# Performance work log

Measured on AMD Instinct MI355X. Metric: run time of the kernel, lower is better.

Reference implementation:

```python
import jax, jax.numpy as jnp
import numpy as np

N = 100000   # nodes
E = 300000   # edges per snapshot
S = 5        # snapshots
D_IN = 128   # node_dim
H = 256      # hidden dim
P = 10000    # post nodes


def setup_inputs() -> dict:
    key = jax.random.key(0)
    ks = jax.random.split(key, 8)
    node_features = jax.random.normal(ks[0], (N, D_IN), jnp.float32)
    edge_index = jax.random.randint(ks[1], (S, 2, E), 0, N, dtype=jnp.int64)
    post_idx = jax.random.randint(ks[2], (P,), 0, N, dtype=jnp.int64)
    glorot = lambda k, sh, fan: jax.random.normal(k, sh, jnp.float32) * (1.0 / np.sqrt(fan))
    return {
        'node_features': node_features,
        'edge_index': edge_index,
        'post_idx': post_idx,
        'W1': glorot(ks[3], (D_IN, H), D_IN), 'b1': jnp.zeros((H,), jnp.float32),
        'W2': glorot(ks[4], (H, H), H),       'b2': jnp.zeros((H,), jnp.float32),
        'Wc1': glorot(ks[5], (H, H // 2), H), 'bc1': jnp.zeros((H // 2,), jnp.float32),
        'Wc2': glorot(ks[6], (H // 2, 1), H // 2), 'bc2': jnp.zeros((1,), jnp.float32),
    }


def gcn_conv(x, src, dst, W, b):
    """PyG GCNConv: h = D^-1/2 (A+I) D^-1/2 (x W) + b, aggregate at target (dst)."""
    n = x.shape[0]
    h = x @ W                                   # [n, out]
    loop = jnp.arange(n, dtype=src.dtype)
    src2 = jnp.concatenate([src, loop])          # add self-loops
    dst2 = jnp.concatenate([dst, loop])
    deg = jax.ops.segment_sum(jnp.ones_like(dst2, jnp.float32), dst2, num_segments=n)
    dinv = jnp.where(deg > 0, jax.lax.rsqrt(deg), 0.0)
    norm = dinv[src2] * dinv[dst2]               # [E+n]
    out = jax.ops.segment_sum(h[src2] * norm[:, None], dst2, num_segments=n)
    return out + b


def reference(node_features, edge_index, post_idx, W1, b1, W2, b2, Wc1, bc1, Wc2, bc2):
    embs = []
    for s in range(edge_index.shape[0]):  # loop over fixed small snapshot count
        src, dst = edge_index[s, 0], edge_index[s, 1]
        # layer 0: 128 -> 256, relu, no skip (dims differ)
        x1 = jax.nn.relu(gcn_conv(node_features, src, dst, W1, b1))
        # layer 1 (last): 256 -> 256, no relu, residual skip
        x2 = gcn_conv(x1, src, dst, W2, b2) + x1
        embs.append(x2)
    agg = jnp.mean(jnp.stack(embs, axis=0), axis=0)  # mean over snapshots
    post = agg[post_idx]                             # [P, H]
    logits = jax.nn.relu(post @ Wc1 + bc1) @ Wc2 + bc2
    return jax.nn.sigmoid(logits[:, 0])              # [P]
```

## Files before the change

### kernel.cpp

```cpp
#include <hip/hip_runtime.h>
#include <hip/hip_bf16.h>
#include <math.h>

#define NN 100000
#define NE 300000
#define NS 5
#define DIN 128
#define HID 256
#define NP 10000
#define NB_N 391

#define NBUCK 1024
#define NBUCK_USED 782
#define PBLK 64
#define EPB 19
#define BCAP 2048
#define CAPR 40960
#define NCPAD 16

typedef short s8v __attribute__((ext_vector_type(8)));
typedef float f4v __attribute__((ext_vector_type(4)));

static __device__ __forceinline__ float bf2f(unsigned short u) {
    union { unsigned int i; float f; } v; v.i = ((unsigned int)u) << 16; return v.f;
}
static __device__ __forceinline__ unsigned short f2bf(float f) {
    union { float f; unsigned int i; } v; v.f = f;
    return (unsigned short)((v.i + 0x7fff + ((v.i >> 16) & 1)) >> 16);
}


__global__ void setpost_kernel(const int* __restrict__ post, int* __restrict__ isPost,
                               int* __restrict__ needed) {
    int i = blockIdx.x * 256 + threadIdx.x;
    int s = blockIdx.y;
    if (i < NP) {
        int nd = post[i];
        needed[(size_t)s * NN + nd] = 1;
        if (s == 0) isPost[nd] = 1;
    }
}


__global__ void hist_kernel(const int* __restrict__ EI, int* __restrict__ bhist) {
    __shared__ int h[NBUCK];
    int s = blockIdx.y, b = blockIdx.x, t = threadIdx.x;
    for (int q = t; q < NBUCK; q += 256) h[q] = 0;
    __syncthreads();
    const int* dstp = EI + (size_t)s * 2 * NE + NE;
    int e0 = b * (EPB * 256);
    #pragma unroll
    for (int j = 0; j < EPB; j++) {
        int e = e0 + j * 256 + t;
        if (e < NE) atomicAdd(&h[dstp[e] >> 7], 1);
    }
    __syncthreads();
    for (int q = t; q < NBUCK; q += 256)
        if (h[q]) atomicAdd(&bhist[s * NBUCK + q], h[q]);
}

__global__ void bscan_kernel(const int* __restrict__ bhist, int* __restrict__ bbase,
                             int* __restrict__ bcur) {
    __shared__ int sm[NBUCK];
    int s = blockIdx.x, t = threadIdx.x;
    int v = bhist[s * NBUCK + t];
    sm[t] = v;
    __syncthreads();
    for (int d = 1; d < NBUCK; d <<= 1) {
        int x = (t >= d) ? sm[t - d] : 0;
        __syncthreads();
        sm[t] += x;
        __syncthreads();
    }
    int base = sm[t] - v;
    bbase[s * NBUCK + t] = base;
    bcur[s * NBUCK + t] = base;
}

__global__ void part_kernel(const int* __restrict__ EI, int* __restrict__ bcur,
                            int2* __restrict__ pairs) {
    __shared__ int h[NBUCK];
    __shared__ int base[NBUCK];
    int s = blockIdx.y, b = blockIdx.x, t = threadIdx.x;
    for (int q = t; q < NBUCK; q += 256) h[q] = 0;
    __syncthreads();
    const int* srcp = EI + (size_t)s * 2 * NE;
    const int* dstp = srcp + NE;
    int e0 = b * (EPB * 256);
    int rs[EPB], rd[EPB];
    #pragma unroll
    for (int j = 0; j < EPB; j++) {
        int e = e0 + j * 256 + t;
        if (e < NE) {
            rs[j] = srcp[e];
            rd[j] = dstp[e];
            atomicAdd(&h[rd[j] >> 7], 1);
        } else {
            rd[j] = -1; rs[j] = 0;
        }
    }
    __syncthreads();
    for (int q = t; q < NBUCK; q += 256) {
        int c = h[q];
        base[q] = c ? atomicAdd(&bcur[s * NBUCK + q], c) : 0;
    }
    __syncthreads();
    #pragma unroll
    for (int j = 0; j < EPB; j++) {
        if (rd[j] >= 0) {
            int pos = atomicAdd(&base[rd[j] >> 7], 1);
            pairs[(size_t)s * NE + pos] = make_int2(rs[j], rd[j]);
        }
    }
}

__global__ void bucket_csr_kernel(const int2* __restrict__ pairs, const int* __restrict__ bbase,
                                  const int* __restrict__ bhist, const int* __restrict__ isPost,
                                  int* __restrict__ cnt, int* __restrict__ offs,
                                  float* __restrict__ dinv, int* __restrict__ csr,
                                  int* __restrict__ needed) {
    __shared__ int nh[128];
    __shared__ int noff[128];
    __shared__ int sbuf[BCAP];
    int s = blockIdx.y, b = blockIdx.x, t = threadIdx.x;
    int base = bbase[s * NBUCK + b];
    int count = bhist[s * NBUCK + b];
    if (count > BCAP) count = BCAP;
    if (t < 128) nh[t] = 0;
    __syncthreads();
    const int2* pp = pairs + (size_t)s * NE + base;
    for (int e = t; e < count; e += 256)
        atomicAdd(&nh[pp[e].y & 127], 1);
    __syncthreads();
    if (t < 128) noff[t] = nh[t];
    __syncthreads();
    for (int d = 1; d < 128; d <<= 1) {
        int x = 0;
        if (t < 128 && t >= d) x = noff[t - d];
        __syncthreads();
        if (t < 128) noff[t] += x;
        __syncthreads();
    }
    if (t < 128) {
        int excl = noff[t] - nh[t];
        noff[t] = excl;
        int g = b * 128 + t;
        if (g < NN) {
            int c = nh[t];
            cnt[(size_t)s * NN + g]  = c;
            offs[(size_t)s * NN + g] = base + excl;
            dinv[(size_t)s * NN + g] = rsqrtf((float)(c + 1));
        }
    }
    __syncthreads();
    for (int e = t; e < count; e += 256) {
        int2 pr = pp[e];
        int pos = atomicAdd(&noff[pr.y & 127], 1);
        sbuf[pos] = pr.x;
        if (isPost[pr.y]) needed[(size_t)s * NN + pr.x] = 1;
    }
    __syncthreads();
    for (int e = t; e < count; e += 256)
        csr[(size_t)s * NE + base + e] = sbuf[e];
}


__global__ void compact_kernel(const int* __restrict__ needed, int* __restrict__ ncount,
                               int* __restrict__ list, int* __restrict__ inv) {
    __shared__ int wcnt[4];
    __shared__ int gbase;
    int s = blockIdx.y;
    int i = blockIdx.x * 256 + threadIdx.x;
    int wave = threadIdx.x >> 6, lane = threadIdx.x & 63;
    bool pred = (i < NN) && (needed[(size_t)s * NN + i] != 0);
    unsigned long long mask = __ballot(pred);
    int wc = __popcll(mask);
    if (lane == 0) wcnt[wave] = wc;
    __syncthreads();
    if (threadIdx.x == 0) {
        int tot = wcnt[0] + wcnt[1] + wcnt[2] + wcnt[3];
        gbase = tot ? atomicAdd(&ncount[s * NCPAD], tot) : 0;
    }
    __syncthreads();
    if (pred) {
        int wbase = gbase;
        #pragma unroll
        for (int q = 0; q < 4; q++) if (q < wave) wbase += wcnt[q];
        int rank = __popcll(mask & ((1ull << lane) - 1ull));
        int slot = wbase + rank;
        if (slot < CAPR) {
            list[(size_t)s * NN + slot] = i;
            inv[(size_t)s * NN + i] = slot;
        }
    }
}


__global__ void cvt_kernel(const float* __restrict__ src, unsigned short* __restrict__ dstp, int n4) {
    int i = blockIdx.x * 256 + threadIdx.x;
    if (i < n4) {
        float4 v = *(const float4*)&src[(size_t)i * 4];
        ushort4 o;
        o.x = f2bf(v.x); o.y = f2bf(v.y); o.z = f2bf(v.z); o.w = f2bf(v.w);
        *(ushort4*)&dstp[(size_t)i * 4] = o;
    }
}

__global__ void tw_kernel(const float* __restrict__ W, unsigned short* __restrict__ Wt,
                          int K, int Ncols) {
    int i = blockIdx.x * 256 + threadIdx.x;
    if (i < K * Ncols) {
        int n = i / K, k = i - n * K;
        Wt[i] = f2bf(W[(size_t)k * Ncols + n]);
    }
}


__global__ __launch_bounds__(512) void agg_mm1_kernel(
        const unsigned short* __restrict__ Xb, const unsigned short* __restrict__ W1t,
        const int* __restrict__ ncount, const float* __restrict__ dinvA,
        const int* __restrict__ offsA, const int* __restrict__ cntA,
        const int* __restrict__ csrA, const int* __restrict__ listA,
        const float* __restrict__ b1, unsigned short* __restrict__ x1cA) {
    int s = blockIdx.y;
    int M = ncount[s * NCPAD];
    if (M > CAPR) M = CAPR;
    if (blockIdx.x * 128 >= M) return;
    const float* dinv = dinvA + (size_t)s * NN;
    const int* offs = offsA + (size_t)s * NN;
    const int* cnt  = cntA + (size_t)s * NN;
    const int* csr  = csrA + (size_t)s * NE;
    const int* list = listA + (size_t)s * NN;
    unsigned short* x1c = x1cA + (size_t)s * CAPR * HID;

    __shared__ unsigned short ldsB[256 * 136];
    int tid = threadIdx.x;
    for (int q = tid; q < 256 * 16; q += 512) {
        int n = q >> 4;
        int k8 = (q & 15) * 8;
        *(s8v*)&ldsB[n * 136 + k8] = *(const s8v*)&W1t[n * 128 + k8];
    }
    __syncthreads();

    int wave = tid >> 6, lane = tid & 63, lr = lane & 15, g = lane >> 4;
    int rowbase = blockIdx.x * 128 + wave * 16;
    int arow = rowbase + lr;

    float ga[4][8];
    #pragma unroll
    for (int kk = 0; kk < 4; kk++)
        #pragma unroll
        for (int j = 0; j < 8; j++) ga[kk][j] = 0.f;
    float di = 0.f;

    if (arow < M) {
        int node = list[arow];
        int o = offs[node], c = cnt[node];
        di = dinv[node];
        const unsigned short* rp = Xb + (size_t)node * DIN + g * 8;
        #pragma unroll
        for (int kk = 0; kk < 4; kk++) {
            s8v h = *(const s8v*)(rp + kk * 32);
            #pragma unroll
            for (int j = 0; j < 8; j++) ga[kk][j] = di * bf2f((unsigned short)h[j]);
        }
        for (int k = 0; k < c; k++) {
            int sv = csr[o + k];
            float wgt = dinv[sv];
            const unsigned short* sp = Xb + (size_t)sv * DIN + g * 8;
            #pragma unroll
            for (int kk = 0; kk < 4; kk++) {
                s8v h = *(const s8v*)(sp + kk * 32);
                #pragma unroll
                for (int j = 0; j < 8; j++) ga[kk][j] += wgt * bf2f((unsigned short)h[j]);
            }
        }
    }

    f4v acc[16];
    #pragma unroll
    for (int t8 = 0; t8 < 16; t8++) acc[t8] = (f4v){0.f, 0.f, 0.f, 0.f};
    #pragma unroll
    for (int kk = 0; kk < 4; kk++) {
        s8v a;
        #pragma unroll
        for (int j = 0; j < 8; j++) a[j] = (short)f2bf(ga[kk][j]);
        #pragma unroll
        for (int t8 = 0; t8 < 16; t8++) {
            s8v b = *(const s8v*)&ldsB[(t8 * 16 + lr) * 136 + kk * 32 + g * 8];
            acc[t8] = __builtin_amdgcn_mfma_f32_16x16x32_bf16(a, b, acc[t8], 0, 0, 0);
        }
    }

    int orow0 = rowbase + g * 4;
    #pragma unroll
    for (int r = 0; r < 4; r++) {
        int row = orow0 + r;
        float sc = __shfl(di, g * 4 + r, 64);
        if (row < M) {
            #pragma unroll
            for (int t8 = 0; t8 < 16; t8++) {
                int col = t8 * 16 + lr;
                float v = sc * acc[t8][r] + b1[col];
                x1c[(size_t)row * HID + col] = f2bf(v > 0.f ? v : 0.f);
            }
        }
    }
}


__global__ void z2_kernel(const unsigned short* __restrict__ x1cA, const float* __restrict__ dinvA,
                          const int* __restrict__ offsA, const int* __restrict__ cntA,
                          const int* __restrict__ csrA, const int* __restrict__ invA,
                          const int* __restrict__ post, unsigned short* __restrict__ z2bA) {
    int s = blockIdx.y;
    const unsigned short* x1c = x1cA + (size_t)s * CAPR * HID;
    const float* dinv = dinvA + (size_t)s * NN;
    const int* offs = offsA + (size_t)s * NN;
    const int* cnt  = cntA + (size_t)s * NN;
    const int* csr  = csrA + (size_t)s * NE;
    const int* inv  = invA + (size_t)s * NN;
    unsigned short* z2b = z2bA + (size_t)s * NP * HID;

    int wave = threadIdx.x >> 6, lane = threadIdx.x & 63;
    int eg = lane >> 4, el = lane & 15;
    int p = blockIdx.x * 4 + wave;
    if (p >= NP) return;
    int node = post[p];
    int o = offs[node], c = cnt[node];
    float acc0[8] = {0.f, 0.f, 0.f, 0.f, 0.f, 0.f, 0.f, 0.f};
    float acc1[8] = {0.f, 0.f, 0.f, 0.f, 0.f, 0.f, 0.f, 0.f};
    for (int k = eg; k < c; k += 4) {
        int sv = csr[o + k];
        float wgt = dinv[sv];
        int r = inv[sv];
        const unsigned short* rp = &x1c[(size_t)r * HID + el * 16];
        s8v h0 = *(const s8v*)rp;
        s8v h1 = *(const s8v*)(rp + 8);
        #pragma unroll
        for (int j = 0; j < 8; j++) {
            acc0[j] += wgt * bf2f((unsigned short)h0[j]);
            acc1[j] += wgt * bf2f((unsigned short)h1[j]);
        }
    }
    if (eg == 0) {
        float di = dinv[node];
        int r = inv[node];
        const unsigned short* rp = &x1c[(size_t)r * HID + el * 16];
        s8v h0 = *(const s8v*)rp;
        s8v h1 = *(const s8v*)(rp + 8);
        #pragma unroll
        for (int j = 0; j < 8; j++) {
            acc0[j] += di * bf2f((unsigned short)h0[j]);
            acc1[j] += di * bf2f((unsigned short)h1[j]);
        }
    }
    #pragma unroll
    for (int j = 0; j < 8; j++) {
        acc0[j] += __shfl_xor(acc0[j], 16, 64);
        acc0[j] += __shfl_xor(acc0[j], 32, 64);
        acc1[j] += __shfl_xor(acc1[j], 16, 64);
        acc1[j] += __shfl_xor(acc1[j], 32, 64);
    }
    if (eg == 0) {
        s8v o0, o1;
        #pragma unroll
        for (int j = 0; j < 8; j++) {
            o0[j] = (short)f2bf(acc0[j]);
            o1[j] = (short)f2bf(acc1[j]);
        }
        unsigned short* wp = &z2b[(size_t)p * HID + el * 16];
        *(s8v*)wp = o0;
        *(s8v*)(wp + 8) = o1;
    }
}


__global__ __launch_bounds__(512) void mm2_kernel(
        const unsigned short* __restrict__ z2bA,
        const unsigned short* __restrict__ W2t,
        const float* __restrict__ dinvA,
        const int* __restrict__ post,
        const int* __restrict__ invA,
        const float* __restrict__ b2,
        const unsigned short* __restrict__ x1cA,
        float* __restrict__ aggPA) {
    int s = blockIdx.z;
    const unsigned short* A = z2bA + (size_t)s * NP * HID;
    const float* dinv = dinvA + (size_t)s * NN;
    const int* inv = invA + (size_t)s * NN;
    const unsigned short* x1c = x1cA + (size_t)s * CAPR * HID;
    float* Out = aggPA + (size_t)s * NP * HID;

    __shared__ unsigned short lds[128 * (HID + 8)];
    int tid = threadIdx.x;
    int colbase = blockIdx.y * 128;
    for (int q = tid; q < 128 * 32; q += 512) {
        int n = q >> 5;
        int k8 = (q & 31) * 8;
        *(s8v*)&lds[n * (HID + 8) + k8] = *(const s8v*)&W2t[(size_t)(colbase + n) * HID + k8];
    }
    __syncthreads();

    int wave = tid >> 6, lane = tid & 63, lr = lane & 15, g = lane >> 4;
    int rowbase = blockIdx.x * 128 + wave * 16;
    int arow = rowbase + lr;

    f4v acc[8];
    #pragma unroll
    for (int t = 0; t < 8; t++) acc[t] = (f4v){0.f, 0.f, 0.f, 0.f};

    #pragma unroll
    for (int kk = 0; kk < HID / 32; kk++) {
        s8v a = (s8v){0, 0, 0, 0, 0, 0, 0, 0};
        if (arow < NP) a = *(const s8v*)&A[(size_t)arow * HID + kk * 32 + g * 8];
        #pragma unroll
        for (int t = 0; t < 8; t++) {
            s8v b = *(const s8v*)&lds[(t * 16 + lr) * (HID + 8) + kk * 32 + g * 8];
            acc[t] = __builtin_amdgcn_mfma_f32_16x16x32_bf16(a, b, acc[t], 0, 0, 0);
        }
    }

    int orow0 = rowbase + g * 4;
    #pragma unroll
    for (int r = 0; r < 4; r++) {
        int row = orow0 + r;
        if (row < NP) {
            int nd = post[row];
            float sc = dinv[nd];
            size_t x1row = (size_t)inv[nd] * HID;
            #pragma unroll
            for (int t = 0; t < 8; t++) {
                int col = colbase + t * 16 + lr;
                Out[(size_t)row * HID + col] =
                    sc * acc[t][r] + b2[col] + bf2f(x1c[x1row + col]);
            }
        }
    }
}


__global__ void redcvt_kernel(const float* __restrict__ aggPA, unsigned short* __restrict__ aggPb) {
    int i = blockIdx.x * 256 + threadIdx.x;
    if (i < NP * HID / 4) {
        float4 a = *(const float4*)&aggPA[(size_t)i * 4];
        #pragma unroll
        for (int s = 1; s < NS; s++) {
            float4 b = *(const float4*)&aggPA[(size_t)s * NP * HID + (size_t)i * 4];
            a.x += b.x; a.y += b.y; a.z += b.z; a.w += b.w;
        }
        ushort4 o;
        o.x = f2bf(a.x); o.y = f2bf(a.y); o.z = f2bf(a.z); o.w = f2bf(a.w);
        *(ushort4*)&aggPb[(size_t)i * 4] = o;
    }
}


__global__ void mm3_kernel(const unsigned short* __restrict__ A,
                           const unsigned short* __restrict__ Bt,
                           const float* __restrict__ bias,
                           float* __restrict__ Out) {
    int tid = threadIdx.x;
    int wave = tid >> 6, lane = tid & 63, lr = lane & 15, g = lane >> 4;
    int rowbase = blockIdx.x * 64 + wave * 16;
    int arow = rowbase + lr;

    f4v acc[8];
    #pragma unroll
    for (int t = 0; t < 8; t++) acc[t] = (f4v){0.f, 0.f, 0.f, 0.f};

    #pragma unroll
    for (int kk = 0; kk < HID / 32; kk++) {
        s8v a = (s8v){0, 0, 0, 0, 0, 0, 0, 0};
        if (arow < NP) a = *(const s8v*)&A[(size_t)arow * HID + kk * 32 + g * 8];
        #pragma unroll
        for (int t = 0; t < 8; t++) {
            s8v b = *(const s8v*)&Bt[(size_t)(t * 16 + lr) * HID + kk * 32 + g * 8];
            acc[t] = __builtin_amdgcn_mfma_f32_16x16x32_bf16(a, b, acc[t], 0, 0, 0);
        }
    }

    int orow0 = rowbase + g * 4;
    #pragma unroll
    for (int r = 0; r < 4; r++) {
        int row = orow0 + r;
        if (row < NP) {
            #pragma unroll
            for (int t = 0; t < 8; t++) {
                int col = t * 16 + lr;
                float v = 0.2f * acc[t][r] + bias[col];
                Out[(size_t)row * 128 + col] = v > 0.f ? v : 0.f;
            }
        }
    }
}

__global__ void final_kernel(const float* __restrict__ hid, const float* __restrict__ Wc2,
                             const float* __restrict__ bc2, float* __restrict__ out) {
    int wave = threadIdx.x >> 6;
    int lane = threadIdx.x & 63;
    int p = blockIdx.x * 4 + wave;
    if (p >= NP) return;
    float part = hid[(size_t)p * 128 + lane] * Wc2[lane]
               + hid[(size_t)p * 128 + 64 + lane] * Wc2[64 + lane];
    for (int off = 32; off; off >>= 1) part += __shfl_down(part, off, 64);
    if (lane == 0) out[p] = 1.f / (1.f + expf(-(part + bc2[0])));
}


extern "C" void kernel_launch(void* const* d_in, const int* in_sizes, int n_in,
                              void* d_out, int out_size, void* d_ws, size_t ws_size,
                              hipStream_t stream) {
    const float* X    = (const float*)d_in[0];
    const int*   EI   = (const int*)d_in[1];
    const int*   post = (const int*)d_in[2];
    const float* W1   = (const float*)d_in[3];
    const float* b1   = (const float*)d_in[4];
    const float* W2   = (const float*)d_in[5];
    const float* b2   = (const float*)d_in[6];
    const float* Wc1  = (const float*)d_in[7];
    const float* bc1  = (const float*)d_in[8];
    const float* Wc2  = (const float*)d_in[9];
    const float* bc2  = (const float*)d_in[10];
    float* out = (float*)d_out;

    char* w = (char*)d_ws;
    auto carve = [&](size_t bytes) {
        void* p = (void*)w;
        w += (bytes + 255) & ~(size_t)255;
        return p;
    };
    unsigned short* Xb    = (unsigned short*)carve((size_t)NN * DIN * 2);
    unsigned short* x1c   = (unsigned short*)carve((size_t)NS * CAPR * HID * 2);
    unsigned short* z2b5  = (unsigned short*)carve((size_t)NS * NP * HID * 2);
    float* aggP5          = (float*)carve((size_t)NS * NP * HID * 4);
    unsigned short* aggPb = (unsigned short*)carve((size_t)NP * HID * 2);
    float* hid            = (float*)carve((size_t)NP * 128 * 4);
    unsigned short* W1t   = (unsigned short*)carve((size_t)256 * 128 * 2);
    unsigned short* W2t   = (unsigned short*)carve((size_t)256 * 256 * 2);
    unsigned short* Wc1t  = (unsigned short*)carve((size_t)128 * 256 * 2);
    float* dinv           = (float*)carve((size_t)NS * NN * 4);
    int*   cnt            = (int*)carve((size_t)NS * NN * 4);
    int*   offs           = (int*)carve((size_t)NS * NN * 4);
    int*   needed         = (int*)carve((size_t)NS * NN * 4);
    int*   list           = (int*)carve((size_t)NS * NN * 4);
    int*   inv            = (int*)carve((size_t)NS * NN * 4);
    int*   isPost         = (int*)carve((size_t)NN * 4);
    int*   bhist          = (int*)carve((size_t)NS * NBUCK * 4);
    int*   bbase          = (int*)carve((size_t)NS * NBUCK * 4);
    int*   bcur           = (int*)carve((size_t)NS * NBUCK * 4);
    int*   ncount         = (int*)carve((size_t)NS * NCPAD * 4);
    int*   csr            = (int*)carve((size_t)NS * NE * 4);
    int2*  pairs          = (int2*)x1c;

    hipMemsetAsync(needed, 0, (size_t)NS * NN * 4, stream);
    hipMemsetAsync(isPost, 0, (size_t)NN * 4, stream);
    hipMemsetAsync(bhist, 0, (size_t)NS * NBUCK * 4, stream);
    hipMemsetAsync(ncount, 0, (size_t)NS * NCPAD * 4, stream);

    cvt_kernel<<<(NN * DIN / 4 + 255) / 256, 256, 0, stream>>>(X, Xb, NN * DIN / 4);
    tw_kernel<<<(128 * 256 + 255) / 256, 256, 0, stream>>>(W1, W1t, 128, 256);
    tw_kernel<<<(256 * 256 + 255) / 256, 256, 0, stream>>>(W2, W2t, 256, 256);
    tw_kernel<<<(256 * 128 + 255) / 256, 256, 0, stream>>>(Wc1, Wc1t, 256, 128);
    setpost_kernel<<<dim3((NP + 255) / 256, NS), 256, 0, stream>>>(post, isPost, needed);

    hist_kernel<<<dim3(PBLK, NS), 256, 0, stream>>>(EI, bhist);
    bscan_kernel<<<NS, NBUCK, 0, stream>>>(bhist, bbase, bcur);
    part_kernel<<<dim3(PBLK, NS), 256, 0, stream>>>(EI, bcur, pairs);
    bucket_csr_kernel<<<dim3(NBUCK_USED, NS), 256, 0, stream>>>(pairs, bbase, bhist, isPost,
                                                                cnt, offs, dinv, csr, needed);
    compact_kernel<<<dim3(NB_N, NS), 256, 0, stream>>>(needed, ncount, list, inv);

    agg_mm1_kernel<<<dim3((CAPR + 127) / 128, NS), 512, 0, stream>>>(
        Xb, W1t, ncount, dinv, offs, cnt, csr, list, b1, x1c);
    z2_kernel<<<dim3((NP + 3) / 4, NS), 256, 0, stream>>>(
        x1c, dinv, offs, cnt, csr, inv, post, z2b5);
    mm2_kernel<<<dim3((NP + 127) / 128, 2, NS), 512, 0, stream>>>(
        z2b5, W2t, dinv, post, inv, b2, x1c, aggP5);

    redcvt_kernel<<<(NP * HID / 4 + 255) / 256, 256, 0, stream>>>(aggP5, aggPb);
    mm3_kernel<<<(NP + 63) / 64, 256, 0, stream>>>(aggPb, Wc1t, bc1, hid);
    final_kernel<<<(NP + 3) / 4, 256, 0, stream>>>(hid, Wc2, bc2, out);
}
```

Before: 243.7 us.

## Sort compacted needed-node list by in-degree class and repad W1 LDS stride

Replaces the single-pass ballot compaction with a three-kernel counting sort that groups needed nodes by in-degree (capped at 7), so the rows in each agg_mm1 wave gather similar edge counts and diverge less. It also changes the LDS row stride for W1 from 136 to 130 elements to alter the bank-conflict pattern. The cost is two extra kernel launches and one extra pass over the needed and cnt arrays. A stride of 130 shorts means the 16-byte vector LDS reads are no longer 16-byte aligned, which may split or slow them.

```diff
diff --git a/kernel.cpp b/kernel.cpp
--- a/kernel.cpp
+++ b/kernel.cpp
@@ -17,6 +17,7 @@
 #define BCAP 2048
 #define CAPR 40960
 #define NCPAD 16
+#define LDB 130
 
 typedef short s8v __attribute__((ext_vector_type(8)));
 typedef float f4v __attribute__((ext_vector_type(4)));
@@ -165,29 +166,59 @@
 }
 
 
-__global__ void compact_kernel(const int* __restrict__ needed, int* __restrict__ ncount,
-                               int* __restrict__ list, int* __restrict__ inv) {
-    __shared__ int wcnt[4];
-    __shared__ int gbase;
+__global__ void ccnt_kernel(const int* __restrict__ needed, const int* __restrict__ cntA,
+                            int* __restrict__ ccount) {
+    __shared__ int lcls[8];
     int s = blockIdx.y;
     int i = blockIdx.x * 256 + threadIdx.x;
-    int wave = threadIdx.x >> 6, lane = threadIdx.x & 63;
+    if (threadIdx.x < 8) lcls[threadIdx.x] = 0;
+    __syncthreads();
+    if (i < NN && needed[(size_t)s * NN + i]) {
+        int c = cntA[(size_t)s * NN + i];
+        if (c > 7) c = 7;
+        atomicAdd(&lcls[c], 1);
+    }
+    __syncthreads();
+    if (threadIdx.x < 8 && lcls[threadIdx.x])
+        atomicAdd(&ccount[(s * 8 + threadIdx.x) * NCPAD], lcls[threadIdx.x]);
+}
+
+__global__ void cscan_kernel(const int* __restrict__ ccount, int* __restrict__ ccur,
+                             int* __restrict__ ncount) {
+    int t = threadIdx.x;
+    if (t < NS) {
+        int tot = 0;
+        for (int c = 0; c < 8; c++) {
+            ccur[(t * 8 + c) * NCPAD] = tot;
+            tot += ccount[(t * 8 + c) * NCPAD];
+        }
+        ncount[t * NCPAD] = tot;
+    }
+}
+
+__global__ void cwrite_kernel(const int* __restrict__ needed, const int* __restrict__ cntA,
+                              int* __restrict__ ccur, int* __restrict__ list,
+                              int* __restrict__ inv) {
+    __shared__ int lcls[8];
+    __shared__ int gb[8];
+    int s = blockIdx.y;
+    int i = blockIdx.x * 256 + threadIdx.x;
+    if (threadIdx.x < 8) lcls[threadIdx.x] = 0;
+    __syncthreads();
     bool pred = (i < NN) && (needed[(size_t)s * NN + i] != 0);
-    unsigned long long mask = __ballot(pred);
-    int wc = __popcll(mask);
-    if (lane == 0) wcnt[wave] = wc;
-    __syncthreads();
-    if (threadIdx.x == 0) {
-        int tot = wcnt[0] + wcnt[1] + wcnt[2] + wcnt[3];
-        gbase = tot ? atomicAdd(&ncount[s * NCPAD], tot) : 0;
-    }
-    __syncthreads();
+    int c = 0, my = 0;
     if (pred) {
-        int wbase = gbase;
-        #pragma unroll
-        for (int q = 0; q < 4; q++) if (q < wave) wbase += wcnt[q];
-        int rank = __popcll(mask & ((1ull << lane) - 1ull));
-        int slot = wbase + rank;
+        c = cntA[(size_t)s * NN + i];
+        if (c > 7) c = 7;
+        my = atomicAdd(&lcls[c], 1);
+    }
+    __syncthreads();
+    if (threadIdx.x < 8)
+        gb[threadIdx.x] = lcls[threadIdx.x]
+            ? atomicAdd(&ccur[(s * 8 + threadIdx.x) * NCPAD], lcls[threadIdx.x]) : 0;
+    __syncthreads();
+    if (pred) {
+        int slot = gb[c] + my;
         if (slot < CAPR) {
             list[(size_t)s * NN + slot] = i;
             inv[(size_t)s * NN + i] = slot;
@@ -233,12 +264,12 @@
     const int* list = listA + (size_t)s * NN;
     unsigned short* x1c = x1cA + (size_t)s * CAPR * HID;
 
-    __shared__ unsigned short ldsB[256 * 136];
+    __shared__ unsigned short ldsB[256 * LDB];
     int tid = threadIdx.x;
     for (int q = tid; q < 256 * 16; q += 512) {
         int n = q >> 4;
         int k8 = (q & 15) * 8;
-        *(s8v*)&ldsB[n * 136 + k8] = *(const s8v*)&W1t[n * 128 + k8];
+        *(s8v*)&ldsB[n * LDB + k8] = *(const s8v*)&W1t[n * 128 + k8];
     }
     __syncthreads();
 
@@ -287,7 +318,7 @@
         for (int j = 0; j < 8; j++) a[j] = (short)f2bf(ga[kk][j]);
         #pragma unroll
         for (int t8 = 0; t8 < 16; t8++) {
-            s8v b = *(const s8v*)&ldsB[(t8 * 16 + lr) * 136 + kk * 32 + g * 8];
+            s8v b = *(const s8v*)&ldsB[(t8 * 16 + lr) * LDB + kk * 32 + g * 8];
             acc[t8] = __builtin_amdgcn_mfma_f32_16x16x32_bf16(a, b, acc[t8], 0, 0, 0);
         }
     }
@@ -550,13 +581,15 @@
     int*   bbase          = (int*)carve((size_t)NS * NBUCK * 4);
     int*   bcur           = (int*)carve((size_t)NS * NBUCK * 4);
     int*   ncount         = (int*)carve((size_t)NS * NCPAD * 4);
+    int*   ccount         = (int*)carve((size_t)NS * 8 * NCPAD * 4);
+    int*   ccur           = (int*)carve((size_t)NS * 8 * NCPAD * 4);
     int*   csr            = (int*)carve((size_t)NS * NE * 4);
     int2*  pairs          = (int2*)x1c;
 
     hipMemsetAsync(needed, 0, (size_t)NS * NN * 4, stream);
     hipMemsetAsync(isPost, 0, (size_t)NN * 4, stream);
     hipMemsetAsync(bhist, 0, (size_t)NS * NBUCK * 4, stream);
-    hipMemsetAsync(ncount, 0, (size_t)NS * NCPAD * 4, stream);
+    hipMemsetAsync(ccount, 0, (size_t)NS * 8 * NCPAD * 4, stream);
 
     cvt_kernel<<<(NN * DIN / 4 + 255) / 256, 256, 0, stream>>>(X, Xb, NN * DIN / 4);
     tw_kernel<<<(128 * 256 + 255) / 256, 256, 0, stream>>>(W1, W1t, 128, 256);
@@ -569,7 +602,10 @@
     part_kernel<<<dim3(PBLK, NS), 256, 0, stream>>>(EI, bcur, pairs);
     bucket_csr_kernel<<<dim3(NBUCK_USED, NS), 256, 0, stream>>>(pairs, bbase, bhist, isPost,
                                                                 cnt, offs, dinv, csr, needed);
-    compact_kernel<<<dim3(NB_N, NS), 256, 0, stream>>>(needed, ncount, list, inv);
+
+    ccnt_kernel<<<dim3(NB_N, NS), 256, 0, stream>>>(needed, cnt, ccount);
+    cscan_kernel<<<1, 64, 0, stream>>>(ccount, ccur, ncount);
+    cwrite_kernel<<<dim3(NB_N, NS), 256, 0, stream>>>(needed, cnt, ccur, list, inv);
 
     agg_mm1_kernel<<<dim3((CAPR + 127) / 128, NS), 512, 0, stream>>>(
         Xb, W1t, ncount, dinv, offs, cnt, csr, list, b1, x1c);
```

After: 255.7 us. +4.9%, slower.
